# Optimization experiments

Measured on AMD Instinct MI355X. Metric: run time of the kernel, lower is better.

## Reference

```python
import jax, jax.numpy as jnp
import numpy as np

N = 100000          # atoms
E = 3200000         # edges (avg degree 32)
G = 2000            # molecules in batch
HID = 64            # hidden_channels == num_filters
NG = 50             # num_gaussians
CUTOFF = 10.0
LOG2 = float(np.log(2.0))


def ssp(x):
    # shifted softplus: softplus(x) - log(2)
    return jax.nn.softplus(x) - LOG2


def setup_inputs() -> dict:
    key = jax.random.key(0)
    ks = jax.random.split(key, 24)
    z = jax.random.randint(ks[0], (N,), 0, 100)
    pos = jax.random.uniform(ks[1], (N, 3), dtype=jnp.float32) * 5.0  # distances < cutoff
    batch = jnp.sort(jax.random.randint(ks[2], (N,), 0, G))
    edge_index = jax.random.randint(ks[3], (2, E), 0, N)

    def w(k, *shape):
        fan_in = shape[0]
        return jax.random.normal(k, shape, dtype=jnp.float32) / jnp.sqrt(jnp.float32(fan_in))

    emb = jax.random.normal(ks[4], (100, HID), dtype=jnp.float32)
    L = 3  # num_interactions; stack per-layer params on leading axis
    params = {
        'mlp_w1': w(ks[5], NG, HID)[None].repeat(L, 0) * 0 + jnp.stack([w(jax.random.fold_in(ks[5], i), NG, HID) for i in range(L)]),
        'mlp_b1': jnp.zeros((L, HID), jnp.float32),
        'mlp_w2': jnp.stack([w(jax.random.fold_in(ks[6], i), HID, HID) for i in range(L)]),
        'mlp_b2': jnp.zeros((L, HID), jnp.float32),
        'cf_lin1_w': jnp.stack([w(jax.random.fold_in(ks[7], i), HID, HID) for i in range(L)]),  # no bias
        'cf_lin2_w': jnp.stack([w(jax.random.fold_in(ks[8], i), HID, HID) for i in range(L)]),
        'cf_lin2_b': jnp.zeros((L, HID), jnp.float32),
        'int_lin_w': jnp.stack([w(jax.random.fold_in(ks[9], i), HID, HID) for i in range(L)]),
        'int_lin_b': jnp.zeros((L, HID), jnp.float32),
    }
    out_w1 = w(ks[10], HID, HID // 2)
    out_b1 = jnp.zeros((HID // 2,), jnp.float32)
    out_w2 = w(ks[11], HID // 2, 1)
    out_b2 = jnp.zeros((1,), jnp.float32)
    fin_w = w(ks[12], 1, 1)
    fin_b = jnp.zeros((1,), jnp.float32)
    return dict(z=z, pos=pos, batch=batch, edge_index=edge_index, emb=emb,
                out_w1=out_w1, out_b1=out_b1, out_w2=out_w2, out_b2=out_b2,
                fin_w=fin_w, fin_b=fin_b, **params)


def reference(z, pos, batch, edge_index, emb,
              mlp_w1, mlp_b1, mlp_w2, mlp_b2,
              cf_lin1_w, cf_lin2_w, cf_lin2_b,
              int_lin_w, int_lin_b,
              out_w1, out_b1, out_w2, out_b2, fin_w, fin_b):
    src, dst = edge_index[0], edge_index[1]
    h = emb[z]                                   # [N, 64]
    # edge distances
    d = jnp.linalg.norm(pos[src] - pos[dst], axis=-1)        # [E]
    # Gaussian smearing
    offsets = jnp.linspace(0.0, CUTOFF, NG, dtype=jnp.float32)
    delta = offsets[1] - offsets[0]
    coeff = -0.5 / (delta * delta)
    rbf = jnp.exp(coeff * (d[:, None] - offsets) ** 2)       # [E, 50]
    # cosine cutoff
    C = 0.5 * (jnp.cos(d * (jnp.pi / CUTOFF)) + 1.0)         # [E]

    L = mlp_w1.shape[0]
    for l in range(L):  # small fixed number of interaction blocks
        W = ssp(rbf @ mlp_w1[l] + mlp_b1[l]) @ mlp_w2[l] + mlp_b2[l]  # [E, 64]
        W = W * C[:, None]
        x = h @ cf_lin1_w[l]                                  # [N, 64]
        msg = x[src] * W                                      # [E, 64]
        agg = jax.ops.segment_sum(msg, dst, num_segments=N)   # [N, 64]
        x = agg @ cf_lin2_w[l] + cf_lin2_b[l]
        x = ssp(x)
        x = x @ int_lin_w[l] + int_lin_b[l]
        h = h + x

    h = ssp(h @ out_w1 + out_b1) @ out_w2 + out_b2            # [N, 1]
    out = jax.ops.segment_sum(h, batch, num_segments=G)       # [G, 1]
    return out @ fin_w + fin_b                                # trailing Linear(1,1)
```

## Files before the change

### kernel.cpp

```cpp
#include <hip/hip_runtime.h>
#include <hip/hip_fp16.h>
#include <cstdint>
#include <cstddef>

#define HIDC   64
#define NGAUSS 50
#define NLAYER 3
#define TGRID  8192
#define BSTRIDE 128
#define MAXBUCK 1024
#define CHUNK_E 6656
#define CUTOFF_F 10.0f
#define LOG2_C 0.69314718055994530942f

typedef _Float16 f16x8 __attribute__((ext_vector_type(8)));
typedef float f32x4 __attribute__((ext_vector_type(4)));
#define MFMA16(a, b, c) __builtin_amdgcn_mfma_f32_16x16x32_f16(a, b, c, 0, 0, 0)

__device__ __forceinline__ float sspf(float v) {
  return fmaxf(v, 0.0f) + log1pf(expf(-fabsf(v))) - LOG2_C;
}

__global__ __launch_bounds__(64) void build_table_k(
    const float* __restrict__ mlp_w1, const float* __restrict__ mlp_b1,
    const float* __restrict__ mlp_w2, const float* __restrict__ mlp_b2,
    __half* __restrict__ tabh) {
  int pid = blockIdx.x;
  int l = pid / TGRID;
  int g = pid - l * TGRID;
  int j = threadIdx.x;
  float d = (float)g * (CUTOFF_F / (float)(TGRID - 1));
  __shared__ float rbf_s[NGAUSS];
  __shared__ float hid_s[HIDC];
  const float delta = CUTOFF_F / (float)(NGAUSS - 1);
  const float coeff = -0.5f / (delta * delta);
  if (j < NGAUSS) {
    float t = d - (float)j * delta;
    rbf_s[j] = expf(coeff * t * t);
  }
  __syncthreads();
  const float* w1 = mlp_w1 + (size_t)l * NGAUSS * HIDC;
  float acc = mlp_b1[l * HIDC + j];
#pragma unroll
  for (int k = 0; k < NGAUSS; ++k) acc = fmaf(rbf_s[k], w1[k * HIDC + j], acc);
  hid_s[j] = sspf(acc);
  __syncthreads();
  const float* w2 = mlp_w2 + (size_t)l * HIDC * HIDC;
  float acc2 = mlp_b2[l * HIDC + j];
#pragma unroll
  for (int m = 0; m < HIDC; ++m) acc2 = fmaf(hid_s[m], w2[m * HIDC + j], acc2);
  float C = 0.5f * (cosf(d * (3.14159265358979323846f / CUTOFF_F)) + 1.0f);
  tabh[(size_t)pid * HIDC + j] = __float2half(acc2 * C);
}

__global__ __launch_bounds__(64) void pack_all_k(
    const float* __restrict__ cf1, const float* __restrict__ cf2,
    const float* __restrict__ intw, const float* __restrict__ ow1,
    __half* __restrict__ wpk) {
  int m = blockIdx.x;
  int lane = threadIdx.x;
  const float* src;
  int nc = 64;
  if (m < 3)      src = cf1 + (size_t)m * 4096;
  else if (m < 6) src = cf2 + (size_t)(m - 3) * 4096;
  else if (m < 9) src = intw + (size_t)(m - 6) * 4096;
  else          { src = ow1; nc = 32; }
  __half* dst = wpk + (size_t)m * 4096;
  for (int ct = 0; ct < nc / 16; ++ct)
    for (int kh = 0; kh < 2; ++kh)
      for (int j = 0; j < 8; ++j)
        dst[((ct * 2 + kh) * 64 + lane) * 8 + j] =
            __float2half(src[(kh * 32 + (lane >> 4) * 8 + j) * nc +
                             ct * 16 + (lane & 15)]);
}

__global__ __launch_bounds__(256) void chist_k(
    const int* __restrict__ edst, int* __restrict__ chunk_hist,
    int* __restrict__ bcnt, int E, int nbuck) {
  __shared__ int cnt[MAXBUCK];
  for (int i = threadIdx.x; i < MAXBUCK; i += 256) cnt[i] = 0;
  __syncthreads();
  int c = blockIdx.x;
  int e0 = c * CHUNK_E;
  int e1 = e0 + CHUNK_E; if (e1 > E) e1 = E;
  for (int e = e0 + threadIdx.x; e < e1; e += 256)
    atomicAdd(&cnt[edst[e] >> 7], 1);
  __syncthreads();
  for (int i = threadIdx.x; i < nbuck; i += 256) {
    int v = cnt[i];
    chunk_hist[c * MAXBUCK + i] = v;
    if (v) atomicAdd(&bcnt[i], v);
  }
}

__global__ __launch_bounds__(256) void bscan_k(
    const int* __restrict__ bcnt, int* __restrict__ boff, int nbuck) {
  __shared__ int sbuf[2][256];
  int tid = threadIdx.x;
  int base = tid * 4;
  int v0 = (base + 0 < nbuck) ? bcnt[base + 0] : 0;
  int v1 = (base + 1 < nbuck) ? bcnt[base + 1] : 0;
  int v2 = (base + 2 < nbuck) ? bcnt[base + 2] : 0;
  int v3 = (base + 3 < nbuck) ? bcnt[base + 3] : 0;
  int p0 = v0, p1 = p0 + v1, p2 = p1 + v2, p3 = p2 + v3;
  int pout = 0;
  sbuf[0][tid] = p3;
  __syncthreads();
  for (int off = 1; off < 256; off <<= 1) {
    int pin = pout; pout ^= 1;
    int v = sbuf[pin][tid];
    if (tid >= off) v += sbuf[pin][tid - off];
    sbuf[pout][tid] = v;
    __syncthreads();
  }
  int texc = sbuf[pout][tid] - p3;
  if (base + 0 < nbuck) boff[base + 0] = texc;
  if (base + 1 < nbuck) boff[base + 1] = texc + p0;
  if (base + 2 < nbuck) boff[base + 2] = texc + p1;
  if (base + 3 < nbuck) boff[base + 3] = texc + p2;
}

__global__ __launch_bounds__(256) void cbase_k(
    const int* __restrict__ chunk_hist, const int* __restrict__ boff,
    int* __restrict__ chunk_base, int nchunk) {
  __shared__ int sbuf[2][256];
  int b = blockIdx.x;
  int tid = threadIdx.x;
  int carry = 0;
  for (int t0 = 0; t0 < nchunk; t0 += 256) {
    int t = t0 + tid;
    int v = (t < nchunk) ? chunk_hist[(size_t)t * MAXBUCK + b] : 0;
    int pout = 0;
    sbuf[0][tid] = v;
    __syncthreads();
    for (int off = 1; off < 256; off <<= 1) {
      int pin = pout; pout ^= 1;
      int s = sbuf[pin][tid];
      if (tid >= off) s += sbuf[pin][tid - off];
      sbuf[pout][tid] = s;
      __syncthreads();
    }
    if (t < nchunk)
      chunk_base[(size_t)t * MAXBUCK + b] = boff[b] + carry + sbuf[pout][tid] - v;
    carry += sbuf[pout][255];
    __syncthreads();
  }
}

__global__ __launch_bounds__(512) void cstage_k(
    const int* __restrict__ ei, const float* __restrict__ pos,
    const int* __restrict__ chunk_hist, const int* __restrict__ chunk_base,
    int2* __restrict__ er, int E, int nbuck) {
  __shared__ int stage_a[CHUNK_E];
  __shared__ int stage_b[CHUNK_E];
  __shared__ int loff[MAXBUCK];
  __shared__ int lcur[MAXBUCK];
  int c = blockIdx.x;
  int tid = threadIdx.x;
  const int* hrow = chunk_hist + (size_t)c * MAXBUCK;
  int b0 = tid * 2;
  int v0 = (b0     < nbuck) ? hrow[b0]     : 0;
  int v1 = (b0 + 1 < nbuck) ? hrow[b0 + 1] : 0;
  int p1 = v0 + v1;
  int (*sb)[512] = (int (*)[512])stage_a;
  int pout = 0;
  sb[0][tid] = p1;
  __syncthreads();
  for (int off = 1; off < 512; off <<= 1) {
    int pin = pout; pout ^= 1;
    int v = sb[pin][tid];
    if (tid >= off) v += sb[pin][tid - off];
    sb[pout][tid] = v;
    __syncthreads();
  }
  int texc = sb[pout][tid] - p1;
  loff[b0] = texc;          lcur[b0] = texc;
  loff[b0 + 1] = texc + v0; lcur[b0 + 1] = texc + v0;
  __syncthreads();
  int e0 = c * CHUNK_E;
  int e1 = e0 + CHUNK_E; if (e1 > E) e1 = E;
  for (int e = e0 + tid; e < e1; e += 512) {
    int s = ei[e], t = ei[E + e];
    float dx = pos[3 * s + 0] - pos[3 * t + 0];
    float dy = pos[3 * s + 1] - pos[3 * t + 1];
    float dz = pos[3 * s + 2] - pos[3 * t + 2];
    float d = sqrtf(fmaf(dx, dx, fmaf(dy, dy, dz * dz)));
    float u = d * ((float)(TGRID - 1) / CUTOFF_F);
    int i0 = (int)(u + 0.5f);
    if (i0 > TGRID - 1) i0 = TGRID - 1;
    int b = t >> 7;
    int dl = t & 127;
    int p = atomicAdd(&lcur[b], 1);
    stage_a[p] = s | (dl << 20);
    stage_b[p] = i0 | (b << 13);
  }
  __syncthreads();
  int total = e1 - e0;
  for (int i = tid; i < total; i += 512) {
    int sbv = stage_b[i];
    int b = sbv >> 13;
    int gb = chunk_base[(size_t)c * MAXBUCK + b];
    er[gb + (i - loff[b])] = make_int2(stage_a[i], sbv & 0x1FFF);
  }
}

__global__ __launch_bounds__(256) void bsort_k(
    const int* __restrict__ boff, const int* __restrict__ bcnt,
    const int2* __restrict__ er, int* __restrict__ er2,
    int* __restrict__ rs, int n) {
  __shared__ int dcnt[BSTRIDE];
  __shared__ int lcur[BSTRIDE];
  __shared__ int sc[2][BSTRIDE];
  int b = blockIdx.x;
  int node0 = b << 7;
  int nn = n - node0; if (nn > BSTRIDE) nn = BSTRIDE;
  int tid = threadIdx.x;
  if (tid < BSTRIDE) dcnt[tid] = 0;
  __syncthreads();
  int base = boff[b];
  int cnt = bcnt[b];
  for (int r = tid; r < cnt; r += 256)
    atomicAdd(&dcnt[(unsigned)er[base + r].x >> 20], 1);
  __syncthreads();
  int pout = 0;
  if (tid < BSTRIDE) sc[0][tid] = dcnt[tid];
  __syncthreads();
  for (int off = 1; off < BSTRIDE; off <<= 1) {
    int pin = pout; pout ^= 1;
    if (tid < BSTRIDE) {
      int v = sc[pin][tid];
      if (tid >= off) v += sc[pin][tid - off];
      sc[pout][tid] = v;
    }
    __syncthreads();
  }
  if (tid < BSTRIDE) {
    int start = base + sc[pout][tid] - dcnt[tid];
    lcur[tid] = start;
    if (tid < nn) rs[node0 + tid] = start;
  }
  if (tid == 0 && b == gridDim.x - 1) rs[n] = base + cnt;
  __syncthreads();
  for (int r = tid; r < cnt; r += 256) {
    int2 rec = er[base + r];
    int dl = (unsigned)rec.x >> 20;
    int p = atomicAdd(&lcur[dl], 1);
    er2[p] = (rec.x & 0x1FFFF) | (rec.y << 17);
  }
}


#define LOADB_P(P, Wpk) \
  const f16x8* P##p = (const f16x8*)(Wpk); \
  const f16x8 P##00 = P##p[0 * 64 + lane], P##01 = P##p[1 * 64 + lane]; \
  const f16x8 P##10 = P##p[2 * 64 + lane], P##11 = P##p[3 * 64 + lane]; \
  const f16x8 P##20 = P##p[4 * 64 + lane], P##21 = P##p[5 * 64 + lane]; \
  const f16x8 P##30 = P##p[6 * 64 + lane], P##31 = P##p[7 * 64 + lane];

#define GEMM_PRO \
  const int lane = threadIdx.x & 63; \
  const int r = lane & 15, g = lane >> 4; \
  const int wid = __builtin_amdgcn_readfirstlane( \
      (int)((blockIdx.x * 256 + threadIdx.x) >> 6)); \
  const int nwv = (int)(gridDim.x << 2); \
  const f32x4 z4 = {0.f, 0.f, 0.f, 0.f};

#define MFMA8(P, a0, a1, c0, c1, c2, c3) \
  c0 = MFMA16(a0, P##00, z4); c0 = MFMA16(a1, P##01, c0); \
  c1 = MFMA16(a0, P##10, z4); c1 = MFMA16(a1, P##11, c1); \
  c2 = MFMA16(a0, P##20, z4); c2 = MFMA16(a1, P##21, c2); \
  c3 = MFMA16(a0, P##30, z4); c3 = MFMA16(a1, P##31, c3);

__global__ __launch_bounds__(256, 2) void init_lin_k(
    const int* __restrict__ z, const float* __restrict__ emb,
    const __half* __restrict__ wpk, float* __restrict__ h,
    __half* __restrict__ h16, __half* __restrict__ x, int ntiles, int n) {
  GEMM_PRO
  LOADB_P(B, wpk)
  for (int t = wid; t < ntiles; t += nwv) {
    int node = t * 16 + r;
    int nodec = node < n ? node : n - 1;
    const int zi = z[nodec];
    const float4* ep = (const float4*)(emb + ((size_t)zi << 6));
    float4 ea = ep[g * 2], eb = ep[g * 2 + 1];
    float4 ec = ep[8 + g * 2], ed = ep[8 + g * 2 + 1];
    f16x8 a0, a1;
    a0[0] = (_Float16)ea.x; a0[1] = (_Float16)ea.y;
    a0[2] = (_Float16)ea.z; a0[3] = (_Float16)ea.w;
    a0[4] = (_Float16)eb.x; a0[5] = (_Float16)eb.y;
    a0[6] = (_Float16)eb.z; a0[7] = (_Float16)eb.w;
    a1[0] = (_Float16)ec.x; a1[1] = (_Float16)ec.y;
    a1[2] = (_Float16)ec.z; a1[3] = (_Float16)ec.w;
    a1[4] = (_Float16)ed.x; a1[5] = (_Float16)ed.y;
    a1[6] = (_Float16)ed.z; a1[7] = (_Float16)ed.w;
    if (node < n) {
      float4* hp = (float4*)(h + ((size_t)node << 6) + g * 8);
      hp[0] = ea; hp[1] = eb;
      float4* hp2 = (float4*)(h + ((size_t)node << 6) + 32 + g * 8);
      hp2[0] = ec; hp2[1] = ed;
      *(f16x8*)(h16 + ((size_t)node << 6) + g * 8) = a0;
      *(f16x8*)(h16 + ((size_t)node << 6) + 32 + g * 8) = a1;
    }
    f32x4 c0, c1, c2, c3;
    MFMA8(B, a0, a1, c0, c1, c2, c3)
    const int nb = t * 16 + (g << 2);
#pragma unroll
    for (int q = 0; q < 4; ++q) {
      const int nq = nb + q;
      if (nq < n) {
        __half* o = x + ((size_t)nq << 6) + r;
        o[0]  = __float2half(c0[q]);
        o[16] = __float2half(c1[q]);
        o[32] = __float2half(c2[q]);
        o[48] = __float2half(c3[q]);
      }
    }
  }
}

__global__ __launch_bounds__(256, 2) void upd0_k(
    const __half* __restrict__ aggh, const __half* __restrict__ wpk2,
    const float* __restrict__ b2, const __half* __restrict__ wpk3,
    const float* __restrict__ b3, float* __restrict__ h,
    __half* __restrict__ h16, int ntiles, int n) {
  __shared__ _Float16 lt[4][16][72];
  GEMM_PRO
  const int wslot = threadIdx.x >> 6;
  _Float16 (*T)[72] = lt[wslot];
  LOADB_P(B2, wpk2)
  LOADB_P(B3, wpk3)
  const float q2a = b2[r], q2b = b2[16 + r], q2c = b2[32 + r], q2d = b2[48 + r];
  const float q3a = b3[r], q3b = b3[16 + r], q3c = b3[32 + r], q3d = b3[48 + r];
  for (int t = wid; t < ntiles; t += nwv) {
    int arow = t * 16 + r; if (arow >= n) arow = n - 1;
    const f16x8* Ap = (const f16x8*)(aggh + ((size_t)arow << 6));
    const f16x8 a0 = Ap[g], a1 = Ap[4 + g];
    f32x4 c0, c1, c2, c3;
    MFMA8(B2, a0, a1, c0, c1, c2, c3)
#pragma unroll
    for (int q = 0; q < 4; ++q) {
      T[g * 4 + q][r]      = (_Float16)sspf(c0[q] + q2a);
      T[g * 4 + q][16 + r] = (_Float16)sspf(c1[q] + q2b);
      T[g * 4 + q][32 + r] = (_Float16)sspf(c2[q] + q2c);
      T[g * 4 + q][48 + r] = (_Float16)sspf(c3[q] + q2d);
    }
    const f16x8 t0 = *(const f16x8*)&T[r][g * 8];
    const f16x8 t1 = *(const f16x8*)&T[r][32 + g * 8];
    MFMA8(B3, t0, t1, c0, c1, c2, c3)
    const int nb = t * 16 + (g << 2);
#pragma unroll
    for (int q = 0; q < 4; ++q) {
      const int nq = nb + q;
      if (nq < n) {
        const size_t idx = ((size_t)nq << 6) + r;
        float n0 = h[idx +  0] + c0[q] + q3a;
        float n1 = h[idx + 16] + c1[q] + q3b;
        float n2 = h[idx + 32] + c2[q] + q3c;
        float n3 = h[idx + 48] + c3[q] + q3d;
        h[idx +  0] = n0; h16[idx +  0] = __float2half(n0);
        h[idx + 16] = n1; h16[idx + 16] = __float2half(n1);
        h[idx + 32] = n2; h16[idx + 32] = __float2half(n2);
        h[idx + 48] = n3; h16[idx + 48] = __float2half(n3);
      }
    }
  }
}

__global__ __launch_bounds__(256, 2) void upd1_k(
    const __half* __restrict__ aggh, const __half* __restrict__ wpk2,
    const float* __restrict__ b2, const __half* __restrict__ wpk3,
    const float* __restrict__ b3, float* __restrict__ h,
    __half* __restrict__ h16, const __half* __restrict__ wpkC,
    __half* __restrict__ x, int ntiles, int n) {
  __shared__ _Float16 lt[4][16][72];
  GEMM_PRO
  const int wslot = threadIdx.x >> 6;
  _Float16 (*T)[72] = lt[wslot];
  LOADB_P(B2, wpk2)
  LOADB_P(B3, wpk3)
  LOADB_P(BC, wpkC)
  const float q2a = b2[r], q2b = b2[16 + r], q2c = b2[32 + r], q2d = b2[48 + r];
  const float q3a = b3[r], q3b = b3[16 + r], q3c = b3[32 + r], q3d = b3[48 + r];
  for (int t = wid; t < ntiles; t += nwv) {
    int arow = t * 16 + r; if (arow >= n) arow = n - 1;
    const f16x8* Ap = (const f16x8*)(aggh + ((size_t)arow << 6));
    const f16x8 a0 = Ap[g], a1 = Ap[4 + g];
    f32x4 c0, c1, c2, c3;
    MFMA8(B2, a0, a1, c0, c1, c2, c3)
#pragma unroll
    for (int q = 0; q < 4; ++q) {
      T[g * 4 + q][r]      = (_Float16)sspf(c0[q] + q2a);
      T[g * 4 + q][16 + r] = (_Float16)sspf(c1[q] + q2b);
      T[g * 4 + q][32 + r] = (_Float16)sspf(c2[q] + q2c);
      T[g * 4 + q][48 + r] = (_Float16)sspf(c3[q] + q2d);
    }
    const f16x8 t0 = *(const f16x8*)&T[r][g * 8];
    const f16x8 t1 = *(const f16x8*)&T[r][32 + g * 8];
    MFMA8(B3, t0, t1, c0, c1, c2, c3)
    const int nb = t * 16 + (g << 2);
#pragma unroll
    for (int q = 0; q < 4; ++q) {
      const int nq = nb + q;
      float n0 = 0.f, n1 = 0.f, n2 = 0.f, n3 = 0.f;
      if (nq < n) {
        const size_t idx = ((size_t)nq << 6) + r;
        n0 = h[idx +  0] + c0[q] + q3a;
        n1 = h[idx + 16] + c1[q] + q3b;
        n2 = h[idx + 32] + c2[q] + q3c;
        n3 = h[idx + 48] + c3[q] + q3d;
        h[idx +  0] = n0; h16[idx +  0] = __float2half(n0);
        h[idx + 16] = n1; h16[idx + 16] = __float2half(n1);
        h[idx + 32] = n2; h16[idx + 32] = __float2half(n2);
        h[idx + 48] = n3; h16[idx + 48] = __float2half(n3);
      }
      T[g * 4 + q][r]      = (_Float16)n0;
      T[g * 4 + q][16 + r] = (_Float16)n1;
      T[g * 4 + q][32 + r] = (_Float16)n2;
      T[g * 4 + q][48 + r] = (_Float16)n3;
    }
    const f16x8 h0 = *(const f16x8*)&T[r][g * 8];
    const f16x8 h1 = *(const f16x8*)&T[r][32 + g * 8];
    MFMA8(BC, h0, h1, c0, c1, c2, c3)
#pragma unroll
    for (int q = 0; q < 4; ++q) {
      const int nq = nb + q;
      if (nq < n) {
        __half* o = x + ((size_t)nq << 6) + r;
        o[0]  = __float2half(c0[q]);
        o[16] = __float2half(c1[q]);
        o[32] = __float2half(c2[q]);
        o[48] = __float2half(c3[q]);
      }
    }
  }
}

__global__ __launch_bounds__(256, 4) void outm16_k(
    const __half* __restrict__ h16, const int* __restrict__ batch,
    const __half* __restrict__ wpk, const float* __restrict__ ob1,
    const float* __restrict__ ow2, const float* __restrict__ ob2,
    float* __restrict__ outg, int ntiles, int n) {
  GEMM_PRO
  const f16x8* Bp = (const f16x8*)(wpk);
  const f16x8 b00 = Bp[0 * 64 + lane], b01 = Bp[1 * 64 + lane];
  const f16x8 b10 = Bp[2 * 64 + lane], b11 = Bp[3 * 64 + lane];
  const float b1a = ob1[r], b1b = ob1[16 + r];
  const float w2a = ow2[r], w2b = ow2[16 + r];
  const float b2o = ob2[0];
  for (int t = wid; t < ntiles; t += nwv) {
    int arow = t * 16 + r; if (arow >= n) arow = n - 1;
    const f16x8* Ap = (const f16x8*)(h16 + ((size_t)arow << 6));
    const f16x8 a0 = Ap[g], a1 = Ap[4 + g];
    f32x4 c0 = MFMA16(a0, b00, z4); c0 = MFMA16(a1, b01, c0);
    f32x4 c1 = MFMA16(a0, b10, z4); c1 = MFMA16(a1, b11, c1);
    float v0 = sspf(c0[0] + b1a) * w2a + sspf(c1[0] + b1b) * w2b;
    float v1 = sspf(c0[1] + b1a) * w2a + sspf(c1[1] + b1b) * w2b;
    float v2 = sspf(c0[2] + b1a) * w2a + sspf(c1[2] + b1b) * w2b;
    float v3 = sspf(c0[3] + b1a) * w2a + sspf(c1[3] + b1b) * w2b;
#pragma unroll
    for (int off = 1; off < 16; off <<= 1) {
      v0 += __shfl_xor(v0, off);
      v1 += __shfl_xor(v1, off);
      v2 += __shfl_xor(v2, off);
      v3 += __shfl_xor(v3, off);
    }
    if (r == 0) {
      const int nb = t * 16 + (g << 2);
      if (nb + 0 < n) unsafeAtomicAdd(&outg[batch[nb + 0]], v0 + b2o);
      if (nb + 1 < n) unsafeAtomicAdd(&outg[batch[nb + 1]], v1 + b2o);
      if (nb + 2 < n) unsafeAtomicAdd(&outg[batch[nb + 2]], v2 + b2o);
      if (nb + 3 < n) unsafeAtomicAdd(&outg[batch[nb + 3]], v3 + b2o);
    }
  }
}

__global__ __launch_bounds__(256) void gather_k(
    const int* __restrict__ rs, const int* __restrict__ er,
    const __half* __restrict__ tabh, const __half* __restrict__ x,
    __half* __restrict__ aggh, int n) {
  int j = threadIdx.x & 63;
  int node = (blockIdx.x * 256 + threadIdx.x) >> 6;
  if (node >= n) return;
  int beg = __builtin_amdgcn_readfirstlane(rs[node]);
  int end = __builtin_amdgcn_readfirstlane(rs[node + 1]);
  float acc = 0.0f;
  int k = beg;
  for (; k + 16 <= end; k += 16) {
    int r0 = er[k + 0];
    int r1 = er[k + 1];
    int r2 = er[k + 2];
    int r3 = er[k + 3];
    int r4 = er[k + 4];
    int r5 = er[k + 5];
    int r6 = er[k + 6];
    int r7 = er[k + 7];
    int r8 = er[k + 8];
    int r9 = er[k + 9];
    int rA = er[k + 10];
    int rB = er[k + 11];
    int rC = er[k + 12];
    int rD = er[k + 13];
    int rE = er[k + 14];
    int rF = er[k + 15];
    float t0 = __half2float(tabh[(((size_t)((unsigned)r0 >> 17)) << 6) + j]);
    float t1 = __half2float(tabh[(((size_t)((unsigned)r1 >> 17)) << 6) + j]);
    float t2 = __half2float(tabh[(((size_t)((unsigned)r2 >> 17)) << 6) + j]);
    float t3 = __half2float(tabh[(((size_t)((unsigned)r3 >> 17)) << 6) + j]);
    float t4 = __half2float(tabh[(((size_t)((unsigned)r4 >> 17)) << 6) + j]);
    float t5 = __half2float(tabh[(((size_t)((unsigned)r5 >> 17)) << 6) + j]);
    float t6 = __half2float(tabh[(((size_t)((unsigned)r6 >> 17)) << 6) + j]);
    float t7 = __half2float(tabh[(((size_t)((unsigned)r7 >> 17)) << 6) + j]);
    float t8 = __half2float(tabh[(((size_t)((unsigned)r8 >> 17)) << 6) + j]);
    float t9 = __half2float(tabh[(((size_t)((unsigned)r9 >> 17)) << 6) + j]);
    float tA = __half2float(tabh[(((size_t)((unsigned)rA >> 17)) << 6) + j]);
    float tB = __half2float(tabh[(((size_t)((unsigned)rB >> 17)) << 6) + j]);
    float tC = __half2float(tabh[(((size_t)((unsigned)rC >> 17)) << 6) + j]);
    float tD = __half2float(tabh[(((size_t)((unsigned)rD >> 17)) << 6) + j]);
    float tE = __half2float(tabh[(((size_t)((unsigned)rE >> 17)) << 6) + j]);
    float tF = __half2float(tabh[(((size_t)((unsigned)rF >> 17)) << 6) + j]);
    float x0 = __half2float(x[((size_t)(r0 & 0x1FFFF) << 6) + j]);
    float x1 = __half2float(x[((size_t)(r1 & 0x1FFFF) << 6) + j]);
    float x2 = __half2float(x[((size_t)(r2 & 0x1FFFF) << 6) + j]);
    float x3 = __half2float(x[((size_t)(r3 & 0x1FFFF) << 6) + j]);
    float x4 = __half2float(x[((size_t)(r4 & 0x1FFFF) << 6) + j]);
    float x5 = __half2float(x[((size_t)(r5 & 0x1FFFF) << 6) + j]);
    float x6 = __half2float(x[((size_t)(r6 & 0x1FFFF) << 6) + j]);
    float x7 = __half2float(x[((size_t)(r7 & 0x1FFFF) << 6) + j]);
    float x8 = __half2float(x[((size_t)(r8 & 0x1FFFF) << 6) + j]);
    float x9 = __half2float(x[((size_t)(r9 & 0x1FFFF) << 6) + j]);
    float xA = __half2float(x[((size_t)(rA & 0x1FFFF) << 6) + j]);
    float xB = __half2float(x[((size_t)(rB & 0x1FFFF) << 6) + j]);
    float xC = __half2float(x[((size_t)(rC & 0x1FFFF) << 6) + j]);
    float xD = __half2float(x[((size_t)(rD & 0x1FFFF) << 6) + j]);
    float xE = __half2float(x[((size_t)(rE & 0x1FFFF) << 6) + j]);
    float xF = __half2float(x[((size_t)(rF & 0x1FFFF) << 6) + j]);
    acc = fmaf(x0, t0, acc);
    acc = fmaf(x1, t1, acc);
    acc = fmaf(x2, t2, acc);
    acc = fmaf(x3, t3, acc);
    acc = fmaf(x4, t4, acc);
    acc = fmaf(x5, t5, acc);
    acc = fmaf(x6, t6, acc);
    acc = fmaf(x7, t7, acc);
    acc = fmaf(x8, t8, acc);
    acc = fmaf(x9, t9, acc);
    acc = fmaf(xA, tA, acc);
    acc = fmaf(xB, tB, acc);
    acc = fmaf(xC, tC, acc);
    acc = fmaf(xD, tD, acc);
    acc = fmaf(xE, tE, acc);
    acc = fmaf(xF, tF, acc);
  }
  for (; k + 4 <= end; k += 4) {
    int r0 = er[k + 0];
    int r1 = er[k + 1];
    int r2 = er[k + 2];
    int r3 = er[k + 3];
    float t0 = __half2float(tabh[(((size_t)((unsigned)r0 >> 17)) << 6) + j]);
    float t1 = __half2float(tabh[(((size_t)((unsigned)r1 >> 17)) << 6) + j]);
    float t2 = __half2float(tabh[(((size_t)((unsigned)r2 >> 17)) << 6) + j]);
    float t3 = __half2float(tabh[(((size_t)((unsigned)r3 >> 17)) << 6) + j]);
    float x0 = __half2float(x[((size_t)(r0 & 0x1FFFF) << 6) + j]);
    float x1 = __half2float(x[((size_t)(r1 & 0x1FFFF) << 6) + j]);
    float x2 = __half2float(x[((size_t)(r2 & 0x1FFFF) << 6) + j]);
    float x3 = __half2float(x[((size_t)(r3 & 0x1FFFF) << 6) + j]);
    acc = fmaf(x0, t0, acc);
    acc = fmaf(x1, t1, acc);
    acc = fmaf(x2, t2, acc);
    acc = fmaf(x3, t3, acc);
  }
  for (; k < end; ++k) {
    int r = er[k];
    float t = __half2float(tabh[(((size_t)((unsigned)r >> 17)) << 6) + j]);
    float xv = __half2float(x[((size_t)(r & 0x1FFFF) << 6) + j]);
    acc = fmaf(xv, t, acc);
  }
  aggh[((size_t)node << 6) + j] = __float2half(acc);
}

__global__ __launch_bounds__(256) void final_k(
    const float* __restrict__ outg, const float* __restrict__ fw,
    const float* __restrict__ fb, float* __restrict__ out, int g) {
  int i = blockIdx.x * blockDim.x + threadIdx.x;
  if (i < g) out[i] = fmaf(outg[i], fw[0], fb[0]);
}

extern "C" void kernel_launch(void* const* d_in, const int* in_sizes, int n_in,
                              void* d_out, int out_size, void* d_ws, size_t ws_size,
                              hipStream_t stream) {
  const int*   z      = (const int*)d_in[0];
  const float* pos    = (const float*)d_in[1];
  const int*   batch  = (const int*)d_in[2];
  const int*   ei     = (const int*)d_in[3];
  const float* emb    = (const float*)d_in[4];
  const float* out_w1 = (const float*)d_in[5];
  const float* out_b1 = (const float*)d_in[6];
  const float* out_w2 = (const float*)d_in[7];
  const float* out_b2 = (const float*)d_in[8];
  const float* fin_w  = (const float*)d_in[9];
  const float* fin_b  = (const float*)d_in[10];
  const float* mlp_w1 = (const float*)d_in[11];
  const float* mlp_b1 = (const float*)d_in[12];
  const float* mlp_w2 = (const float*)d_in[13];
  const float* mlp_b2 = (const float*)d_in[14];
  const float* cf1    = (const float*)d_in[15];
  const float* cf2    = (const float*)d_in[16];
  const float* cf2b   = (const float*)d_in[17];
  const float* intw   = (const float*)d_in[18];
  const float* intb   = (const float*)d_in[19];

  const int N = in_sizes[0];
  const int E = in_sizes[3] / 2;
  const int G = out_size;
  const int NBUCK = (N + BSTRIDE - 1) / BSTRIDE;
  const int NCHUNK = (E + CHUNK_E - 1) / CHUNK_E;
  const int NTILES = (N + 15) / 16;
  const int GB = (NTILES + 3) / 4;

  char* wsb = (char*)d_ws;
  size_t off = 0;
  auto alloc = [&](size_t bytes) { char* p = wsb + off; off += (bytes + 255) & ~(size_t)255; return p; };
  float*   h     = (float*)alloc((size_t)N * HIDC * sizeof(float));
  __half*  h16   = (__half*)alloc((size_t)N * HIDC * sizeof(__half));
  __half*  x     = (__half*)alloc((size_t)N * HIDC * sizeof(__half));
  __half*  aggh  = (__half*)alloc((size_t)N * HIDC * sizeof(__half));
  __half*  tabh  = (__half*)alloc((size_t)NLAYER * TGRID * HIDC * sizeof(__half));
  __half*  wpk   = (__half*)alloc((size_t)10 * 4096 * sizeof(__half));
  int2*    er    = (int2*)alloc((size_t)E * sizeof(int2));
  int*     er2   = (int*)alloc((size_t)E * sizeof(int));
  int*     rs    = (int*)alloc((size_t)(N + 1) * sizeof(int));
  int*     bcnt  = (int*)alloc((size_t)MAXBUCK * sizeof(int));
  int*     boff  = (int*)alloc((size_t)MAXBUCK * sizeof(int));
  int*     chist = (int*)alloc((size_t)NCHUNK * MAXBUCK * sizeof(int));
  int*     cbase = (int*)alloc((size_t)NCHUNK * MAXBUCK * sizeof(int));
  float*   outg  = (float*)alloc((size_t)G * sizeof(float));

  build_table_k<<<dim3(NLAYER * TGRID), dim3(64), 0, stream>>>(
      mlp_w1, mlp_b1, mlp_w2, mlp_b2, tabh);
  pack_all_k<<<dim3(10), dim3(64), 0, stream>>>(cf1, cf2, intw, out_w1, wpk);
  (void)hipMemsetAsync(outg, 0, (size_t)G * sizeof(float), stream);
  (void)hipMemsetAsync(bcnt, 0, (size_t)MAXBUCK * sizeof(int), stream);
  chist_k<<<dim3(NCHUNK), dim3(256), 0, stream>>>(ei + E, chist, bcnt, E, NBUCK);
  bscan_k<<<dim3(1), dim3(256), 0, stream>>>(bcnt, boff, NBUCK);
  cbase_k<<<dim3(NBUCK), dim3(256), 0, stream>>>(chist, boff, cbase, NCHUNK);
  cstage_k<<<dim3(NCHUNK), dim3(512), 0, stream>>>(
      ei, pos, chist, cbase, er, E, NBUCK);
  bsort_k<<<dim3(NBUCK), dim3(256), 0, stream>>>(boff, bcnt, er, er2, rs, N);
  init_lin_k<<<dim3(GB), dim3(256), 0, stream>>>(
      z, emb, wpk, h, h16, x, NTILES, N);

  const int gather_blocks = (N + 3) / 4;
  for (int l = 0; l < NLAYER; ++l) {
    gather_k<<<dim3(gather_blocks), dim3(256), 0, stream>>>(
        rs, er2, tabh + (size_t)l * TGRID * HIDC, x, aggh, N);
    if (l < NLAYER - 1) {
      upd1_k<<<dim3(GB), dim3(256), 0, stream>>>(
          aggh, wpk + (size_t)(3 + l) * 4096, cf2b + l * HIDC,
          wpk + (size_t)(6 + l) * 4096, intb + l * HIDC, h, h16,
          wpk + (size_t)(l + 1) * 4096, x, NTILES, N);
    } else {
      upd0_k<<<dim3(GB), dim3(256), 0, stream>>>(
          aggh, wpk + (size_t)(3 + l) * 4096, cf2b + l * HIDC,
          wpk + (size_t)(6 + l) * 4096, intb + l * HIDC, h, h16, NTILES, N);
    }
  }

  outm16_k<<<dim3(GB), dim3(256), 0, stream>>>(
      h16, batch, wpk + (size_t)9 * 4096, out_b1, out_w2, out_b2, outg, NTILES, N);
  final_k<<<dim3((G + 255) / 256), dim3(256), 0, stream>>>(
      outg, fin_w, fin_b, (float*)d_out, G);
}
```

Measured before the change: 545.9 us.

## Fuse output head into final interaction update kernel and halve update grid

The last-layer update kernel now computes the output MLP head and the per-molecule atomic readout directly from the updated hidden state, staged through shared memory. This removes the separate output kernel launch and the write and re-read of h and h16 for the final layer. The grid for the init and update kernels is also halved, so each wave handles two tiles, which cuts block count but reduces parallel slack.

```diff
diff --git a/kernel.cpp b/kernel.cpp
--- a/kernel.cpp
+++ b/kernel.cpp
@@ -318,19 +318,28 @@
   }
 }
 
-__global__ __launch_bounds__(256, 2) void upd0_k(
+__global__ __launch_bounds__(256, 2) void updF_k(
     const __half* __restrict__ aggh, const __half* __restrict__ wpk2,
     const float* __restrict__ b2, const __half* __restrict__ wpk3,
-    const float* __restrict__ b3, float* __restrict__ h,
-    __half* __restrict__ h16, int ntiles, int n) {
+    const float* __restrict__ b3, const float* __restrict__ h,
+    const int* __restrict__ batch, const __half* __restrict__ wpkO,
+    const float* __restrict__ ob1, const float* __restrict__ ow2,
+    const float* __restrict__ ob2, float* __restrict__ outg,
+    int ntiles, int n) {
   __shared__ _Float16 lt[4][16][72];
   GEMM_PRO
   const int wslot = threadIdx.x >> 6;
   _Float16 (*T)[72] = lt[wslot];
   LOADB_P(B2, wpk2)
   LOADB_P(B3, wpk3)
+  const f16x8* Op = (const f16x8*)(wpkO);
+  const f16x8 O00 = Op[0 * 64 + lane], O01 = Op[1 * 64 + lane];
+  const f16x8 O10 = Op[2 * 64 + lane], O11 = Op[3 * 64 + lane];
   const float q2a = b2[r], q2b = b2[16 + r], q2c = b2[32 + r], q2d = b2[48 + r];
   const float q3a = b3[r], q3b = b3[16 + r], q3c = b3[32 + r], q3d = b3[48 + r];
+  const float b1a = ob1[r], b1b = ob1[16 + r];
+  const float w2a = ow2[r], w2b = ow2[16 + r];
+  const float b2o = ob2[0];
   for (int t = wid; t < ntiles; t += nwv) {
     int arow = t * 16 + r; if (arow >= n) arow = n - 1;
     const f16x8* Ap = (const f16x8*)(aggh + ((size_t)arow << 6));
@@ -351,17 +360,39 @@
 #pragma unroll
     for (int q = 0; q < 4; ++q) {
       const int nq = nb + q;
+      float n0 = 0.f, n1 = 0.f, n2 = 0.f, n3 = 0.f;
       if (nq < n) {
         const size_t idx = ((size_t)nq << 6) + r;
-        float n0 = h[idx +  0] + c0[q] + q3a;
-        float n1 = h[idx + 16] + c1[q] + q3b;
-        float n2 = h[idx + 32] + c2[q] + q3c;
-        float n3 = h[idx + 48] + c3[q] + q3d;
-        h[idx +  0] = n0; h16[idx +  0] = __float2half(n0);
-        h[idx + 16] = n1; h16[idx + 16] = __float2half(n1);
-        h[idx + 32] = n2; h16[idx + 32] = __float2half(n2);
-        h[idx + 48] = n3; h16[idx + 48] = __float2half(n3);
+        n0 = h[idx +  0] + c0[q] + q3a;
+        n1 = h[idx + 16] + c1[q] + q3b;
+        n2 = h[idx + 32] + c2[q] + q3c;
+        n3 = h[idx + 48] + c3[q] + q3d;
       }
+      T[g * 4 + q][r]      = (_Float16)n0;
+      T[g * 4 + q][16 + r] = (_Float16)n1;
+      T[g * 4 + q][32 + r] = (_Float16)n2;
+      T[g * 4 + q][48 + r] = (_Float16)n3;
+    }
+    const f16x8 h0 = *(const f16x8*)&T[r][g * 8];
+    const f16x8 h1 = *(const f16x8*)&T[r][32 + g * 8];
+    c0 = MFMA16(h0, O00, z4); c0 = MFMA16(h1, O01, c0);
+    c1 = MFMA16(h0, O10, z4); c1 = MFMA16(h1, O11, c1);
+    float v0 = sspf(c0[0] + b1a) * w2a + sspf(c1[0] + b1b) * w2b;
+    float v1 = sspf(c0[1] + b1a) * w2a + sspf(c1[1] + b1b) * w2b;
+    float v2 = sspf(c0[2] + b1a) * w2a + sspf(c1[2] + b1b) * w2b;
+    float v3 = sspf(c0[3] + b1a) * w2a + sspf(c1[3] + b1b) * w2b;
+#pragma unroll
+    for (int off = 1; off < 16; off <<= 1) {
+      v0 += __shfl_xor(v0, off);
+      v1 += __shfl_xor(v1, off);
+      v2 += __shfl_xor(v2, off);
+      v3 += __shfl_xor(v3, off);
+    }
+    if (r == 0) {
+      if (nb + 0 < n) unsafeAtomicAdd(&outg[batch[nb + 0]], v0 + b2o);
+      if (nb + 1 < n) unsafeAtomicAdd(&outg[batch[nb + 1]], v1 + b2o);
+      if (nb + 2 < n) unsafeAtomicAdd(&outg[batch[nb + 2]], v2 + b2o);
+      if (nb + 3 < n) unsafeAtomicAdd(&outg[batch[nb + 3]], v3 + b2o);
     }
   }
 }
@@ -431,45 +462,6 @@
         o[32] = __float2half(c2[q]);
         o[48] = __float2half(c3[q]);
       }
-    }
-  }
-}
-
-__global__ __launch_bounds__(256, 4) void outm16_k(
-    const __half* __restrict__ h16, const int* __restrict__ batch,
-    const __half* __restrict__ wpk, const float* __restrict__ ob1,
-    const float* __restrict__ ow2, const float* __restrict__ ob2,
-    float* __restrict__ outg, int ntiles, int n) {
-  GEMM_PRO
-  const f16x8* Bp = (const f16x8*)(wpk);
-  const f16x8 b00 = Bp[0 * 64 + lane], b01 = Bp[1 * 64 + lane];
-  const f16x8 b10 = Bp[2 * 64 + lane], b11 = Bp[3 * 64 + lane];
-  const float b1a = ob1[r], b1b = ob1[16 + r];
-  const float w2a = ow2[r], w2b = ow2[16 + r];
-  const float b2o = ob2[0];
-  for (int t = wid; t < ntiles; t += nwv) {
-    int arow = t * 16 + r; if (arow >= n) arow = n - 1;
-    const f16x8* Ap = (const f16x8*)(h16 + ((size_t)arow << 6));
-    const f16x8 a0 = Ap[g], a1 = Ap[4 + g];
-    f32x4 c0 = MFMA16(a0, b00, z4); c0 = MFMA16(a1, b01, c0);
-    f32x4 c1 = MFMA16(a0, b10, z4); c1 = MFMA16(a1, b11, c1);
-    float v0 = sspf(c0[0] + b1a) * w2a + sspf(c1[0] + b1b) * w2b;
-    float v1 = sspf(c0[1] + b1a) * w2a + sspf(c1[1] + b1b) * w2b;
-    float v2 = sspf(c0[2] + b1a) * w2a + sspf(c1[2] + b1b) * w2b;
-    float v3 = sspf(c0[3] + b1a) * w2a + sspf(c1[3] + b1b) * w2b;
-#pragma unroll
-    for (int off = 1; off < 16; off <<= 1) {
-      v0 += __shfl_xor(v0, off);
-      v1 += __shfl_xor(v1, off);
-      v2 += __shfl_xor(v2, off);
-      v3 += __shfl_xor(v3, off);
-    }
-    if (r == 0) {
-      const int nb = t * 16 + (g << 2);
-      if (nb + 0 < n) unsafeAtomicAdd(&outg[batch[nb + 0]], v0 + b2o);
-      if (nb + 1 < n) unsafeAtomicAdd(&outg[batch[nb + 1]], v1 + b2o);
-      if (nb + 2 < n) unsafeAtomicAdd(&outg[batch[nb + 2]], v2 + b2o);
-      if (nb + 3 < n) unsafeAtomicAdd(&outg[batch[nb + 3]], v3 + b2o);
     }
   }
 }
@@ -615,7 +607,7 @@
   const int NBUCK = (N + BSTRIDE - 1) / BSTRIDE;
   const int NCHUNK = (E + CHUNK_E - 1) / CHUNK_E;
   const int NTILES = (N + 15) / 16;
-  const int GB = (NTILES + 3) / 4;
+  const int GBU = (NTILES + 7) / 8;
 
   char* wsb = (char*)d_ws;
   size_t off = 0;
@@ -646,7 +638,7 @@
   cstage_k<<<dim3(NCHUNK), dim3(512), 0, stream>>>(
       ei, pos, chist, cbase, er, E, NBUCK);
   bsort_k<<<dim3(NBUCK), dim3(256), 0, stream>>>(boff, bcnt, er, er2, rs, N);
-  init_lin_k<<<dim3(GB), dim3(256), 0, stream>>>(
+  init_lin_k<<<dim3(GBU), dim3(256), 0, stream>>>(
       z, emb, wpk, h, h16, x, NTILES, N);
 
   const int gather_blocks = (N + 3) / 4;
@@ -654,19 +646,19 @@
     gather_k<<<dim3(gather_blocks), dim3(256), 0, stream>>>(
         rs, er2, tabh + (size_t)l * TGRID * HIDC, x, aggh, N);
     if (l < NLAYER - 1) {
-      upd1_k<<<dim3(GB), dim3(256), 0, stream>>>(
+      upd1_k<<<dim3(GBU), dim3(256), 0, stream>>>(
           aggh, wpk + (size_t)(3 + l) * 4096, cf2b + l * HIDC,
           wpk + (size_t)(6 + l) * 4096, intb + l * HIDC, h, h16,
           wpk + (size_t)(l + 1) * 4096, x, NTILES, N);
     } else {
-      upd0_k<<<dim3(GB), dim3(256), 0, stream>>>(
+      updF_k<<<dim3(GBU), dim3(256), 0, stream>>>(
           aggh, wpk + (size_t)(3 + l) * 4096, cf2b + l * HIDC,
-          wpk + (size_t)(6 + l) * 4096, intb + l * HIDC, h, h16, NTILES, N);
-    }
-  }
-
-  outm16_k<<<dim3(GB), dim3(256), 0, stream>>>(
-      h16, batch, wpk + (size_t)9 * 4096, out_b1, out_w2, out_b2, outg, NTILES, N);
+          wpk + (size_t)(6 + l) * 4096, intb + l * HIDC, h,
+          batch, wpk + (size_t)9 * 4096, out_b1, out_w2, out_b2, outg,
+          NTILES, N);
+    }
+  }
+
   final_k<<<dim3((G + 255) / 256), dim3(256), 0, stream>>>(
       outg, fin_w, fin_b, (float*)d_out, G);
 }
```

New measurement: 566.9 us. +3.9%, slower.
